# Optimization experiments

Measured on AMD Instinct MI355X. Metric: run time of the kernel, lower is better.

Reference implementation:

```python
import jax, jax.numpy as jnp
import numpy as np

EPS = 1e-12  # matches torch.nn.functional.normalize eps


def _l2_normalize(x):
    n = jnp.linalg.norm(x, axis=-1, keepdims=True)
    return x / jnp.maximum(n, EPS)


def setup_inputs() -> dict:
    key = jax.random.key(0)
    k1, k2, k3, k4 = jax.random.split(key, 4)
    N, D = 8192, 1024
    return {
        "query_ids": jax.random.randint(k1, (N,), 0, 1000, dtype=jnp.int64 if jax.config.jax_enable_x64 else jnp.int32),
        "key_ids": jax.random.randint(k2, (N,), 0, 1000, dtype=jnp.int64 if jax.config.jax_enable_x64 else jnp.int32),
        "query_embed": jax.random.normal(k3, (N, D), dtype=jnp.float32),
        "key_embed": jax.random.normal(k4, (N, D), dtype=jnp.float32),
        "k": 5,
    }


def reference(query_ids, key_ids, query_embed, key_embed, k):
    q = _l2_normalize(query_embed)          # [N, D]
    kb = _l2_normalize(key_embed)           # [N, D]
    sims = q @ kb.T                          # [N, N] cosine similarities
    # argsort(descending)[1:k+1] == top-(k+1) indices, dropping the best match
    _, idx = jax.lax.top_k(sims, k + 1)      # [N, k+1]
    idx = idx[:, 1:]                         # [N, k]
    matched = (key_ids[idx] == query_ids[:, None]).astype(jnp.float32)  # [N, k]
    # mean over k per row, then mean over rows == global mean (equal row sizes)
    return jnp.mean(matched)
```

## Files before the change

kernel.cpp:

```cpp
#include <hip/hip_runtime.h>
#include <math.h>

#define NROWS 8192
#define DIM   1024
#define KDIM  1024
#define KSEL  5
#define TOPK  6
#define QB    128
#define KBB   256
#define NKB   (NROWS / KBB)
#define NQB   (NROWS / QB)
#define PS    51

typedef __attribute__((ext_vector_type(8))) short bf16x8;
typedef __attribute__((ext_vector_type(4))) float f32x4;


__device__ __forceinline__ unsigned short f2bf(float x) {
    unsigned u = __float_as_uint(x);
    unsigned r = (u + 0x7fffu + ((u >> 16) & 1u)) >> 16;
    return (unsigned short)r;
}

__device__ __forceinline__ bool better(float v, int id, float v2, int id2) {
    return (v > v2) || (v == v2 && id < id2);
}
__device__ __forceinline__ void insert6(float v, int id, float* tv, int* ti) {
    if (!better(v, id, tv[TOPK - 1], ti[TOPK - 1])) return;
    int j = TOPK - 1;
    while (j > 0 && better(v, id, tv[j - 1], ti[j - 1])) {
        tv[j] = tv[j - 1]; ti[j] = ti[j - 1]; --j;
    }
    tv[j] = v; ti[j] = id;
}

__device__ __forceinline__ void ins6(float v, int id, float* tv, int* ti) {
    if (v <= tv[5]) return;
    bool gt[6];
#pragma unroll
    for (int j = 0; j < 6; ++j) gt[j] = v > tv[j];
#pragma unroll
    for (int j = 5; j >= 1; --j)
        if (gt[j - 1]) { tv[j] = tv[j - 1]; ti[j] = ti[j - 1]; }
    if (gt[0]) { tv[0] = v; ti[0] = id; }
#pragma unroll
    for (int j = 1; j < 6; ++j)
        if (gt[j] && !gt[j - 1]) { tv[j] = v; ti[j] = id; }
}

__device__ __forceinline__ void async16(const unsigned short* g, unsigned short* l) {
    __builtin_amdgcn_global_load_lds(
        (const __attribute__((address_space(1))) void*)g,
        (__attribute__((address_space(3))) void*)l, 16, 0, 0);
}

__global__ __launch_bounds__(128) void prep_kernel(
        const float* __restrict__ q, const float* __restrict__ kb,
        unsigned short* __restrict__ Q2, unsigned short* __restrict__ K2) {
    const int b = blockIdx.x;
    const bool isQ = (b < NROWS);
    const int r = isQ ? b : b - NROWS;
    const float* src = (isQ ? q : kb) + (size_t)r * DIM;
    unsigned short* D = (isQ ? Q2 : K2) + (size_t)r * KDIM;

    const int t = threadIdx.x;
    float4 v0 = *(const float4*)(src + t * 4);
    float4 v1 = *(const float4*)(src + 512 + t * 4);
    float s = v0.x * v0.x + v0.y * v0.y + v0.z * v0.z + v0.w * v0.w
            + v1.x * v1.x + v1.y * v1.y + v1.z * v1.z + v1.w * v1.w;
    for (int o = 32; o; o >>= 1) s += __shfl_down(s, o, 64);
    __shared__ float wsum[2];
    __shared__ float inv_s;
    int lane = t & 63, wid = t >> 6;
    if (lane == 0) wsum[wid] = s;
    __syncthreads();
    if (t == 0)
        inv_s = 1.0f / fmaxf(sqrtf(wsum[0] + wsum[1]), 1e-12f);
    __syncthreads();
    const float inv = inv_s;

    float xs[8] = {v0.x * inv, v0.y * inv, v0.z * inv, v0.w * inv,
                   v1.x * inv, v1.y * inv, v1.z * inv, v1.w * inv};
    bf16x8 hi;
#pragma unroll
    for (int i = 0; i < 8; ++i)
        hi[i] = (short)f2bf(xs[i]);
    const int off = (t >> 3) * 64 + (((t & 7) ^ (r & 7)) * 8);
    *(bf16x8*)(D + off) = hi;
}

__global__ __launch_bounds__(256, 2) void gemm_topk_kernel(
        const unsigned short* __restrict__ Q2, const unsigned short* __restrict__ K2,
        float2* __restrict__ partials) {
    __shared__ __align__(16) char smem[53248];
    unsigned short* Ks = (unsigned short*)smem;
    unsigned short* Qs = Ks + KBB * 64;
    float2* mbuf = (float2*)smem;

    const int tid = threadIdx.x;
    const int w = tid >> 6, l = tid & 63;
    const int l15 = l & 15, l4 = l >> 4;
    const int qbase = blockIdx.x * QB;
    const int kbase = blockIdx.y * KBB;
    const int wkh = w & 1;
    const int wqh = w >> 1;

    const int arow  = tid >> 3;
    const int akoff = (tid & 7) * 8;

    const int xr = l15 & 7;
    const int fa_row = (wkh * 128 + l15) * 64;
    const int fb_row = (wqh * 64 + l15) * 64;

    const size_t qstage = (size_t)(qbase + arow) * KDIM + akoff;
    const size_t kstage = (size_t)(kbase + arow) * KDIM + akoff;

    f32x4 acc[8][4];
#pragma unroll
    for (int mt = 0; mt < 8; ++mt)
#pragma unroll
        for (int nt = 0; nt < 4; ++nt) acc[mt][nt] = (f32x4){0.f, 0.f, 0.f, 0.f};

#pragma unroll 1
    for (int k0 = 0; k0 < KDIM; k0 += 64) {
#pragma unroll
        for (int j = 0; j < 8; ++j)
            async16(K2 + kstage + (size_t)j * 32 * KDIM + k0,
                    Ks + (tid + j * 256) * 8);
#pragma unroll
        for (int j = 0; j < 4; ++j)
            async16(Q2 + qstage + (size_t)j * 32 * KDIM + k0,
                    Qs + (tid + j * 256) * 8);
        __syncthreads();
#pragma unroll
        for (int ks = 0; ks < 2; ++ks) {
            const int p8 = ((ks * 4 + l4) ^ xr) * 8;
            bf16x8 af[8], bf[4];
#pragma unroll
            for (int mt = 0; mt < 8; ++mt)
                af[mt] = *(const bf16x8*)(Ks + fa_row + mt * 1024 + p8);
#pragma unroll
            for (int nt = 0; nt < 4; ++nt)
                bf[nt] = *(const bf16x8*)(Qs + fb_row + nt * 1024 + p8);
#pragma unroll
            for (int mt = 0; mt < 8; ++mt)
#pragma unroll
                for (int nt = 0; nt < 4; ++nt)
                    acc[mt][nt] = __builtin_amdgcn_mfma_f32_16x16x32_bf16(
                        af[mt], bf[nt], acc[mt][nt], 0, 0, 0);
        }
        __syncthreads();
    }

    float tvl[4][6]; int til[4][6];
#pragma unroll
    for (int n = 0; n < 4; ++n)
#pragma unroll
        for (int i = 0; i < 6; ++i) { tvl[n][i] = -INFINITY; til[n][i] = 0x7fffffff; }

#pragma unroll
    for (int nt = 0; nt < 4; ++nt) {
#pragma unroll
        for (int mt = 0; mt < 8; ++mt) {
            const f32x4 a = acc[mt][nt];
            const float m4 = fmaxf(fmaxf(a.x, a.y), fmaxf(a.z, a.w));
            if (m4 > tvl[nt][5]) {
                const int kk = kbase + wkh * 128 + mt * 16 + l4 * 4;
                ins6(a.x, kk + 0, tvl[nt], til[nt]);
                ins6(a.y, kk + 1, tvl[nt], til[nt]);
                ins6(a.z, kk + 2, tvl[nt], til[nt]);
                ins6(a.w, kk + 3, tvl[nt], til[nt]);
            }
        }
    }

    __syncthreads();
    const int slot = wkh * 4 + l4;
#pragma unroll
    for (int nt = 0; nt < 4; ++nt) {
        const int ql = wqh * 64 + nt * 16 + l15;
        float2* dst = mbuf + (size_t)ql * PS + slot * 6;
#pragma unroll
        for (int e = 0; e < 6; ++e)
            dst[e] = make_float2(tvl[nt][e], __int_as_float(til[nt][e]));
    }
    __syncthreads();

    if (tid < 128) {
        float tv[6]; int ti[6];
#pragma unroll
        for (int i = 0; i < 6; ++i) { tv[i] = -INFINITY; ti[i] = 0x7fffffff; }
        const float2* src = mbuf + (size_t)tid * PS;
        for (int e = 0; e < 48; ++e) {
            float2 p = src[e];
            if (p.x < tv[5]) continue;
            insert6(p.x, __float_as_int(p.y), tv, ti);
        }
        size_t off = ((size_t)(qbase + tid) * NKB + blockIdx.y) * TOPK;
#pragma unroll
        for (int i = 0; i < 6; ++i)
            partials[off + i] = make_float2(tv[i], __int_as_float(ti[i]));
    }
}

__global__ __launch_bounds__(256) void merge_kernel(
        const float2* __restrict__ partials,
        const int* __restrict__ query_ids, const int* __restrict__ key_ids,
        int* __restrict__ counter, int* __restrict__ done,
        float* __restrict__ out) {
    __shared__ float2 lbuf[32][49];
    __shared__ int sc[32];
    const int tid  = threadIdx.x;
    const int rloc = tid >> 3;
    const int part = tid & 7;
    const int row  = blockIdx.x * 32 + rloc;

    float tv[6]; int ti[6];
#pragma unroll
    for (int i = 0; i < 6; ++i) { tv[i] = -INFINITY; ti[i] = 0x7fffffff; }
    const float2* src = partials + ((size_t)row * NKB + part * 4) * TOPK;
#pragma unroll
    for (int e = 0; e < 24; ++e) {
        float2 p = src[e];
        if (p.x < tv[5]) continue;
        insert6(p.x, __float_as_int(p.y), tv, ti);
    }
#pragma unroll
    for (int i = 0; i < 6; ++i)
        lbuf[rloc][part * 6 + i] = make_float2(tv[i], __int_as_float(ti[i]));
    __syncthreads();

    if (part == 0) {
        float tv2[6]; int ti2[6];
#pragma unroll
        for (int i = 0; i < 6; ++i) { tv2[i] = -INFINITY; ti2[i] = 0x7fffffff; }
#pragma unroll
        for (int e = 0; e < 48; ++e) {
            float2 p = lbuf[rloc][e];
            if (p.x < tv2[5]) continue;
            insert6(p.x, __float_as_int(p.y), tv2, ti2);
        }
        const int qid = query_ids[row];
        int cnt = 0;
#pragma unroll
        for (int r = 1; r < TOPK; ++r)
            cnt += (key_ids[ti2[r]] == qid) ? 1 : 0;
        sc[rloc] = cnt;
    }
    __syncthreads();
    if (tid == 0) {
        int c = 0;
#pragma unroll
        for (int i = 0; i < 32; ++i) c += sc[i];
        atomicAdd(counter, c);
        __threadfence();
        int prev = atomicAdd(done, 1);
        if (prev == gridDim.x - 1) {
            int total = atomicAdd(counter, 0);
            out[0] = (float)total / (float)(NROWS * KSEL);
        }
    }
}

extern "C" void kernel_launch(void* const* d_in, const int* in_sizes, int n_in,
                              void* d_out, int out_size, void* d_ws, size_t ws_size,
                              hipStream_t stream) {
    (void)in_sizes; (void)n_in; (void)out_size; (void)ws_size;
    const int*   query_ids = (const int*)d_in[0];
    const int*   key_ids   = (const int*)d_in[1];
    const float* q         = (const float*)d_in[2];
    const float* kb        = (const float*)d_in[3];

    char* ws = (char*)d_ws;
    const size_t MB16 = (size_t)NROWS * KDIM * sizeof(unsigned short);
    int*            counter  = (int*)ws;
    unsigned short* Q2       = (unsigned short*)(ws + 256);
    unsigned short* K2       = (unsigned short*)(ws + 256 + MB16);
    float2*         partials = (float2*)(ws + 256 + 2 * MB16);

    hipMemsetAsync(counter, 0, 2 * sizeof(int), stream);
    prep_kernel<<<2 * NROWS, 128, 0, stream>>>(q, kb, Q2, K2);
    gemm_topk_kernel<<<dim3(NQB, NKB), 256, 0, stream>>>(Q2, K2, partials);
    merge_kernel<<<NROWS / 32, 256, 0, stream>>>(partials, query_ids, key_ids,
                                                 counter, counter + 1,
                                                 (float*)d_out);
}
```

Baseline: 350.8 us.

## Double-buffer LDS tiles with 256-row query block and 512 threads

The query tile per block doubles to 256 rows, run by 512 threads (8 waves). Shared memory becomes two 64KB ping-pong buffers, so the next k-slice's async loads are issued before the MFMA work on the current slice, and one barrier per iteration is removed. MFMA sections are wrapped in s_setprio to favour matrix issue. The 128KB LDS footprint allows at most one block per CU, so latency hiding now relies on the overlap within a block rather than on multiple resident blocks.

```diff
diff --git a/kernel.cpp b/kernel.cpp
--- a/kernel.cpp
+++ b/kernel.cpp
@@ -6,7 +6,7 @@
 #define KDIM  1024
 #define KSEL  5
 #define TOPK  6
-#define QB    128
+#define QB    256
 #define KBB   256
 #define NKB   (NROWS / KBB)
 #define NQB   (NROWS / QB)
@@ -89,12 +89,10 @@
     *(bf16x8*)(D + off) = hi;
 }
 
-__global__ __launch_bounds__(256, 2) void gemm_topk_kernel(
+__global__ __launch_bounds__(512, 2) void gemm_topk_kernel(
         const unsigned short* __restrict__ Q2, const unsigned short* __restrict__ K2,
         float2* __restrict__ partials) {
-    __shared__ __align__(16) char smem[53248];
-    unsigned short* Ks = (unsigned short*)smem;
-    unsigned short* Qs = Ks + KBB * 64;
+    __shared__ __align__(16) char smem[131072];
     float2* mbuf = (float2*)smem;
 
     const int tid = threadIdx.x;
@@ -121,35 +119,62 @@
 #pragma unroll
         for (int nt = 0; nt < 4; ++nt) acc[mt][nt] = (f32x4){0.f, 0.f, 0.f, 0.f};
 
+    {
+        unsigned short* Ksb = (unsigned short*)smem;
+        unsigned short* Qsb = Ksb + 16384;
+#pragma unroll
+        for (int j = 0; j < 4; ++j)
+            async16(K2 + kstage + (size_t)j * 64 * KDIM,
+                    Ksb + (tid + j * 512) * 8);
+#pragma unroll
+        for (int j = 0; j < 4; ++j)
+            async16(Q2 + qstage + (size_t)j * 64 * KDIM,
+                    Qsb + (tid + j * 512) * 8);
+    }
+    __syncthreads();
+
+    int cur = 0;
 #pragma unroll 1
     for (int k0 = 0; k0 < KDIM; k0 += 64) {
-#pragma unroll
-        for (int j = 0; j < 8; ++j)
-            async16(K2 + kstage + (size_t)j * 32 * KDIM + k0,
-                    Ks + (tid + j * 256) * 8);
-#pragma unroll
-        for (int j = 0; j < 4; ++j)
-            async16(Q2 + qstage + (size_t)j * 32 * KDIM + k0,
-                    Qs + (tid + j * 256) * 8);
-        __syncthreads();
+        unsigned short* Ksb = (unsigned short*)(smem + (cur << 16));
+        unsigned short* Qsb = Ksb + 16384;
+
+        const int nk0 = k0 + 64;
+        if (nk0 < KDIM) {
+            unsigned short* Ksn = (unsigned short*)(smem + ((cur ^ 1) << 16));
+            unsigned short* Qsn = Ksn + 16384;
+#pragma unroll
+            for (int j = 0; j < 4; ++j)
+                async16(K2 + kstage + (size_t)j * 64 * KDIM + nk0,
+                        Ksn + (tid + j * 512) * 8);
+#pragma unroll
+            for (int j = 0; j < 4; ++j)
+                async16(Q2 + qstage + (size_t)j * 64 * KDIM + nk0,
+                        Qsn + (tid + j * 512) * 8);
+        }
+
 #pragma unroll
         for (int ks = 0; ks < 2; ++ks) {
             const int p8 = ((ks * 4 + l4) ^ xr) * 8;
-            bf16x8 af[8], bf[4];
+            bf16x8 af[8], bfr[4];
 #pragma unroll
             for (int mt = 0; mt < 8; ++mt)
-                af[mt] = *(const bf16x8*)(Ks + fa_row + mt * 1024 + p8);
+                af[mt] = *(const bf16x8*)(Ksb + fa_row + mt * 1024 + p8);
 #pragma unroll
             for (int nt = 0; nt < 4; ++nt)
-                bf[nt] = *(const bf16x8*)(Qs + fb_row + nt * 1024 + p8);
+                bfr[nt] = *(const bf16x8*)(Qsb + fb_row + nt * 1024 + p8);
+            __builtin_amdgcn_s_setprio(1);
 #pragma unroll
             for (int mt = 0; mt < 8; ++mt)
 #pragma unroll
                 for (int nt = 0; nt < 4; ++nt)
                     acc[mt][nt] = __builtin_amdgcn_mfma_f32_16x16x32_bf16(
-                        af[mt], bf[nt], acc[mt][nt], 0, 0, 0);
-        }
+                        af[mt], bfr[nt], acc[mt][nt], 0, 0, 0);
+            __builtin_amdgcn_s_setprio(0);
+        }
+
         __syncthreads();
+        cur ^= 1;
     }
 
     float tvl[4][6]; int til[4][6];
@@ -186,7 +211,7 @@
     }
     __syncthreads();
 
-    if (tid < 128) {
+    if (tid < 256) {
         float tv[6]; int ti[6];
 #pragma unroll
         for (int i = 0; i < 6; ++i) { tv[i] = -INFINITY; ti[i] = 0x7fffffff; }
@@ -280,7 +305,7 @@
 
     hipMemsetAsync(counter, 0, 2 * sizeof(int), stream);
     prep_kernel<<<2 * NROWS, 128, 0, stream>>>(q, kb, Q2, K2);
-    gemm_topk_kernel<<<dim3(NQB, NKB), 256, 0, stream>>>(Q2, K2, partials);
+    gemm_topk_kernel<<<dim3(NQB, NKB), 512, 0, stream>>>(Q2, K2, partials);
     merge_kernel<<<NROWS / 32, 256, 0, stream>>>(partials, query_ids, key_ids,
                                                  counter, counter + 1,
                                                  (float*)d_out);
```

Measured after the change: 353.2 us. No clear change (+0.7%).

## Double-buffer K tiles, load Q fragments directly to registers, widen GEMM block

Applied to the files above, without the earlier changes.

The GEMM kernel moves to 512 threads covering 256 queries per block. K tiles are double-buffered in LDS with async loads for the next k-step issued before the current MFMAs. Q fragments are fetched straight from global memory into registers one step ahead, dropping the Q LDS staging. MFMA issue is wrapped with s_setprio, and the top-k reduction now runs in two halves. The prep kernel processes one row per wave with no block-level sync. This aims to hide global-load latency and cut LDS traffic, at the cost of more registers and uncoalesced-ish direct global Q loads.

```diff
diff --git a/kernel.cpp b/kernel.cpp
--- a/kernel.cpp
+++ b/kernel.cpp
@@ -6,10 +6,11 @@
 #define KDIM  1024
 #define KSEL  5
 #define TOPK  6
-#define QB    128
+#define QB    256
 #define KBB   256
 #define NKB   (NROWS / KBB)
 #define NQB   (NROWS / QB)
+#define NT    (KDIM / 64)
 #define PS    51
 
 typedef __attribute__((ext_vector_type(8))) short bf16x8;
@@ -54,47 +55,50 @@
         (__attribute__((address_space(3))) void*)l, 16, 0, 0);
 }
 
-__global__ __launch_bounds__(128) void prep_kernel(
+__global__ __launch_bounds__(256) void prep_kernel(
         const float* __restrict__ q, const float* __restrict__ kb,
         unsigned short* __restrict__ Q2, unsigned short* __restrict__ K2) {
-    const int b = blockIdx.x;
+    const int w = threadIdx.x >> 6, lane = threadIdx.x & 63;
+    const int b = blockIdx.x * 4 + w;
     const bool isQ = (b < NROWS);
     const int r = isQ ? b : b - NROWS;
     const float* src = (isQ ? q : kb) + (size_t)r * DIM;
     unsigned short* D = (isQ ? Q2 : K2) + (size_t)r * KDIM;
 
-    const int t = threadIdx.x;
-    float4 v0 = *(const float4*)(src + t * 4);
-    float4 v1 = *(const float4*)(src + 512 + t * 4);
-    float s = v0.x * v0.x + v0.y * v0.y + v0.z * v0.z + v0.w * v0.w
-            + v1.x * v1.x + v1.y * v1.y + v1.z * v1.z + v1.w * v1.w;
+    float4 v[4];
+#pragma unroll
+    for (int i = 0; i < 4; ++i)
+        v[i] = *(const float4*)(src + i * 256 + lane * 4);
+
+    float s = 0.f;
+#pragma unroll
+    for (int i = 0; i < 4; ++i)
+        s += v[i].x * v[i].x + v[i].y * v[i].y + v[i].z * v[i].z + v[i].w * v[i].w;
     for (int o = 32; o; o >>= 1) s += __shfl_down(s, o, 64);
-    __shared__ float wsum[2];
-    __shared__ float inv_s;
-    int lane = t & 63, wid = t >> 6;
-    if (lane == 0) wsum[wid] = s;
-    __syncthreads();
-    if (t == 0)
-        inv_s = 1.0f / fmaxf(sqrtf(wsum[0] + wsum[1]), 1e-12f);
-    __syncthreads();
-    const float inv = inv_s;
-
-    float xs[8] = {v0.x * inv, v0.y * inv, v0.z * inv, v0.w * inv,
-                   v1.x * inv, v1.y * inv, v1.z * inv, v1.w * inv};
-    bf16x8 hi;
-#pragma unroll
-    for (int i = 0; i < 8; ++i)
-        hi[i] = (short)f2bf(xs[i]);
-    const int off = (t >> 3) * 64 + (((t & 7) ^ (r & 7)) * 8);
-    *(bf16x8*)(D + off) = hi;
-}
-
-__global__ __launch_bounds__(256, 2) void gemm_topk_kernel(
+    s = __shfl(s, 0, 64);
+    const float inv = 1.0f / fmaxf(sqrtf(s), 1e-12f);
+
+    bf16x8 g0, g1;
+    g0[0] = (short)f2bf(v[0].x * inv); g0[1] = (short)f2bf(v[0].y * inv);
+    g0[2] = (short)f2bf(v[0].z * inv); g0[3] = (short)f2bf(v[0].w * inv);
+    g0[4] = (short)f2bf(v[2].x * inv); g0[5] = (short)f2bf(v[2].y * inv);
+    g0[6] = (short)f2bf(v[2].z * inv); g0[7] = (short)f2bf(v[2].w * inv);
+    g1[0] = (short)f2bf(v[1].x * inv); g1[1] = (short)f2bf(v[1].y * inv);
+    g1[2] = (short)f2bf(v[1].z * inv); g1[3] = (short)f2bf(v[1].w * inv);
+    g1[4] = (short)f2bf(v[3].x * inv); g1[5] = (short)f2bf(v[3].y * inv);
+    g1[6] = (short)f2bf(v[3].z * inv); g1[7] = (short)f2bf(v[3].w * inv);
+
+    const int perm = ((lane & 7) ^ (r & 7)) * 8;
+    const int off0 = (lane >> 3) * 64 + perm;
+    const int off1 = (8 + (lane >> 3)) * 64 + perm;
+    *(bf16x8*)(D + off0) = g0;
+    *(bf16x8*)(D + off1) = g1;
+}
+
+__global__ __launch_bounds__(512, 2) void gemm_topk_kernel(
         const unsigned short* __restrict__ Q2, const unsigned short* __restrict__ K2,
         float2* __restrict__ partials) {
-    __shared__ __align__(16) char smem[53248];
-    unsigned short* Ks = (unsigned short*)smem;
-    unsigned short* Qs = Ks + KBB * 64;
+    __shared__ __align__(16) char smem[65536];
     float2* mbuf = (float2*)smem;
 
     const int tid = threadIdx.x;
@@ -105,15 +109,20 @@
     const int wkh = w & 1;
     const int wqh = w >> 1;
 
-    const int arow  = tid >> 3;
     const int akoff = (tid & 7) * 8;
-
     const int xr = l15 & 7;
     const int fa_row = (wkh * 128 + l15) * 64;
-    const int fb_row = (wqh * 64 + l15) * 64;
-
-    const size_t qstage = (size_t)(qbase + arow) * KDIM + akoff;
-    const size_t kstage = (size_t)(kbase + arow) * KDIM + akoff;
+
+    const size_t kstage = (size_t)(kbase + (tid >> 3)) * KDIM + akoff;
+
+    unsigned qv[2][4];
+#pragma unroll
+    for (int ks = 0; ks < 2; ++ks)
+#pragma unroll
+        for (int nt = 0; nt < 4; ++nt) {
+            const int qrow = qbase + wqh * 64 + nt * 16 + l15;
+            qv[ks][nt] = (unsigned)qrow * KDIM + (unsigned)(((ks * 4 + l4) ^ xr) * 8);
+        }
 
     f32x4 acc[8][4];
 #pragma unroll
@@ -121,36 +130,73 @@
 #pragma unroll
         for (int nt = 0; nt < 4; ++nt) acc[mt][nt] = (f32x4){0.f, 0.f, 0.f, 0.f};
 
+    unsigned short* Kb0 = (unsigned short*)smem;
+    unsigned short* Kb1 = (unsigned short*)(smem + 32768);
+
+    bf16x8 b0[2][4], b1[2][4];
+
+#pragma unroll
+    for (int j = 0; j < 4; ++j)
+        async16(K2 + kstage + (size_t)j * 64 * KDIM, Kb0 + (tid + j * 512) * 8);
+#pragma unroll
+    for (int ks = 0; ks < 2; ++ks)
+#pragma unroll
+        for (int nt = 0; nt < 4; ++nt)
+            b0[ks][nt] = *(const bf16x8*)(Q2 + qv[ks][nt]);
+    __syncthreads();
+
+#define STEP(TT, CURBUF, NXTBUF, BC, BN)                                      \
+    {                                                                         \
+        const int tt = (TT);                                                  \
+        if (tt + 1 < NT) {                                                    \
+            const size_t nk0 = (size_t)(tt + 1) * 64;                         \
+            _Pragma("unroll")                                                 \
+            for (int j = 0; j < 4; ++j)                                       \
+                async16(K2 + kstage + (size_t)j * 64 * KDIM + nk0,            \
+                        (NXTBUF) + (tid + j * 512) * 8);                      \
+            _Pragma("unroll")                                                 \
+            for (int ks = 0; ks < 2; ++ks)                                    \
+                _Pragma("unroll")                                             \
+                for (int nt = 0; nt < 4; ++nt)                                \
+                    (BN)[ks][nt] = *(const bf16x8*)(Q2 + qv[ks][nt] +         \
+                                                    (unsigned)(tt + 1) * 64); \
+        }                                                                     \
+        _Pragma("unroll")                                                     \
+        for (int ks = 0; ks < 2; ++ks) {                                      \
+            const int p8 = ((ks * 4 + l4) ^ xr) * 8;                          \
+            bf16x8 af[4];                                                     \
+            _Pragma("unroll")                                                 \
+            for (int m = 0; m < 4; ++m)                                       \
+                af[m] = *(const bf16x8*)((CURBUF) + fa_row + m * 1024 + p8);  \
+            __builtin_amdgcn_s_setprio(1);                                    \
+            _Pragma("unroll")                                                 \
+            for (int m = 0; m < 4; ++m)                                       \
+                _Pragma("unroll")                                             \
+                for (int nt = 0; nt < 4; ++nt)                                \
+                    acc[m][nt] = __builtin_amdgcn_mfma_f32_16x16x32_bf16(     \
+                        af[m], (BC)[ks][nt], acc[m][nt], 0, 0, 0);            \
+            __builtin_amdgcn_s_setprio(0);                                    \
+            _Pragma("unroll")                                                 \
+            for (int m = 0; m < 4; ++m)                                       \
+                af[m] = *(const bf16x8*)((CURBUF) + fa_row + (m + 4) * 1024 + p8); \
+            __builtin_amdgcn_s_setprio(1);                                    \
+            _Pragma("unroll")                                                 \
+            for (int m = 0; m < 4; ++m)                                       \
+                _Pragma("unroll")                                             \
+                for (int nt = 0; nt < 4; ++nt)                                \
+                    acc[m + 4][nt] = __builtin_amdgcn_mfma_f32_16x16x32_bf16( \
+                        af[m], (BC)[ks][nt], acc[m + 4][nt], 0, 0, 0);        \
+            __builtin_amdgcn_s_setprio(0);                                    \
+        }                                                                     \
+        __syncthreads();        \
+    }
+
 #pragma unroll 1
-    for (int k0 = 0; k0 < KDIM; k0 += 64) {
-#pragma unroll
-        for (int j = 0; j < 8; ++j)
-            async16(K2 + kstage + (size_t)j * 32 * KDIM + k0,
-                    Ks + (tid + j * 256) * 8);
-#pragma unroll
-        for (int j = 0; j < 4; ++j)
-            async16(Q2 + qstage + (size_t)j * 32 * KDIM + k0,
-                    Qs + (tid + j * 256) * 8);
-        __syncthreads();
-#pragma unroll
-        for (int ks = 0; ks < 2; ++ks) {
-            const int p8 = ((ks * 4 + l4) ^ xr) * 8;
-            bf16x8 af[8], bf[4];
-#pragma unroll
-            for (int mt = 0; mt < 8; ++mt)
-                af[mt] = *(const bf16x8*)(Ks + fa_row + mt * 1024 + p8);
-#pragma unroll
-            for (int nt = 0; nt < 4; ++nt)
-                bf[nt] = *(const bf16x8*)(Qs + fb_row + nt * 1024 + p8);
-#pragma unroll
-            for (int mt = 0; mt < 8; ++mt)
-#pragma unroll
-                for (int nt = 0; nt < 4; ++nt)
-                    acc[mt][nt] = __builtin_amdgcn_mfma_f32_16x16x32_bf16(
-                        af[mt], bf[nt], acc[mt][nt], 0, 0, 0);
-        }
-        __syncthreads();
-    }
+    for (int t2 = 0; t2 < NT; t2 += 2) {
+        STEP(t2,     Kb0, Kb1, b0, b1);
+        STEP(t2 + 1, Kb1, Kb0, b1, b0);
+    }
+#undef STEP
 
     float tvl[4][6]; int til[4][6];
 #pragma unroll
@@ -174,32 +220,36 @@
         }
     }
 
-    __syncthreads();
     const int slot = wkh * 4 + l4;
-#pragma unroll
-    for (int nt = 0; nt < 4; ++nt) {
-        const int ql = wqh * 64 + nt * 16 + l15;
-        float2* dst = mbuf + (size_t)ql * PS + slot * 6;
-#pragma unroll
-        for (int e = 0; e < 6; ++e)
-            dst[e] = make_float2(tvl[nt][e], __int_as_float(til[nt][e]));
-    }
-    __syncthreads();
-
-    if (tid < 128) {
-        float tv[6]; int ti[6];
-#pragma unroll
-        for (int i = 0; i < 6; ++i) { tv[i] = -INFINITY; ti[i] = 0x7fffffff; }
-        const float2* src = mbuf + (size_t)tid * PS;
-        for (int e = 0; e < 48; ++e) {
-            float2 p = src[e];
-            if (p.x < tv[5]) continue;
-            insert6(p.x, __float_as_int(p.y), tv, ti);
-        }
-        size_t off = ((size_t)(qbase + tid) * NKB + blockIdx.y) * TOPK;
-#pragma unroll
-        for (int i = 0; i < 6; ++i)
-            partials[off + i] = make_float2(tv[i], __int_as_float(ti[i]));
+#pragma unroll 1
+    for (int h = 0; h < 2; ++h) {
+        if ((wqh >> 1) == h) {
+#pragma unroll
+            for (int nt = 0; nt < 4; ++nt) {
+                const int ql = (wqh & 1) * 64 + nt * 16 + l15;
+                float2* dst = mbuf + (size_t)ql * PS + slot * 6;
+#pragma unroll
+                for (int e = 0; e < 6; ++e)
+                    dst[e] = make_float2(tvl[nt][e], __int_as_float(til[nt][e]));
+            }
+        }
+        __syncthreads();
+        if (tid < 128) {
+            float tv[6]; int ti[6];
+#pragma unroll
+            for (int i = 0; i < 6; ++i) { tv[i] = -INFINITY; ti[i] = 0x7fffffff; }
+            const float2* src = mbuf + (size_t)tid * PS;
+            for (int e = 0; e < 48; ++e) {
+                float2 p = src[e];
+                if (p.x < tv[5]) continue;
+                insert6(p.x, __float_as_int(p.y), tv, ti);
+            }
+            size_t off = ((size_t)(qbase + h * 128 + tid) * NKB + blockIdx.y) * TOPK;
+#pragma unroll
+            for (int i = 0; i < 6; ++i)
+                partials[off + i] = make_float2(tv[i], __int_as_float(ti[i]));
+        }
+        __syncthreads();
     }
 }
 
@@ -279,8 +329,8 @@
     float2*         partials = (float2*)(ws + 256 + 2 * MB16);
 
     hipMemsetAsync(counter, 0, 2 * sizeof(int), stream);
-    prep_kernel<<<2 * NROWS, 128, 0, stream>>>(q, kb, Q2, K2);
-    gemm_topk_kernel<<<dim3(NQB, NKB), 256, 0, stream>>>(Q2, K2, partials);
+    prep_kernel<<<(2 * NROWS) / 4, 256, 0, stream>>>(q, kb, Q2, K2);
+    gemm_topk_kernel<<<dim3(NQB, NKB), 512, 0, stream>>>(Q2, K2, partials);
     merge_kernel<<<NROWS / 32, 256, 0, stream>>>(partials, query_ids, key_ids,
                                                  counter, counter + 1,
                                                  (float*)d_out);
```

After: 731.5 us. +108.5%, slower.

## Load GEMM fragments directly from global memory, drop LDS staging and barriers

Applied to the files above, without the earlier changes.

The GEMM main loop no longer stages Q and K tiles into shared memory with async loads and block barriers. Each wave now reads its bf16 MFMA fragments straight from global memory through L2/L1, and raises wave priority around the MFMA bursts. The prep kernel is also reworked so one wave normalizes one row, which removes the shared-memory reduction and its syncthreads. The trade is that operands once shared through LDS are now re-read from cache by several waves, and global-load latency is exposed per k-step with no software pipelining.

```diff
diff --git a/kernel.cpp b/kernel.cpp
--- a/kernel.cpp
+++ b/kernel.cpp
@@ -10,6 +10,7 @@
 #define KBB   256
 #define NKB   (NROWS / KBB)
 #define NQB   (NROWS / QB)
+#define NT    (KDIM / 64)
 #define PS    51
 
 typedef __attribute__((ext_vector_type(8))) short bf16x8;
@@ -48,54 +49,50 @@
         if (gt[j] && !gt[j - 1]) { tv[j] = v; ti[j] = id; }
 }
 
-__device__ __forceinline__ void async16(const unsigned short* g, unsigned short* l) {
-    __builtin_amdgcn_global_load_lds(
-        (const __attribute__((address_space(1))) void*)g,
-        (__attribute__((address_space(3))) void*)l, 16, 0, 0);
-}
-
-__global__ __launch_bounds__(128) void prep_kernel(
+__global__ __launch_bounds__(256) void prep_kernel(
         const float* __restrict__ q, const float* __restrict__ kb,
         unsigned short* __restrict__ Q2, unsigned short* __restrict__ K2) {
-    const int b = blockIdx.x;
+    const int w = threadIdx.x >> 6, lane = threadIdx.x & 63;
+    const int b = blockIdx.x * 4 + w;
     const bool isQ = (b < NROWS);
     const int r = isQ ? b : b - NROWS;
     const float* src = (isQ ? q : kb) + (size_t)r * DIM;
     unsigned short* D = (isQ ? Q2 : K2) + (size_t)r * KDIM;
 
-    const int t = threadIdx.x;
-    float4 v0 = *(const float4*)(src + t * 4);
-    float4 v1 = *(const float4*)(src + 512 + t * 4);
-    float s = v0.x * v0.x + v0.y * v0.y + v0.z * v0.z + v0.w * v0.w
-            + v1.x * v1.x + v1.y * v1.y + v1.z * v1.z + v1.w * v1.w;
+    float4 v[4];
+#pragma unroll
+    for (int i = 0; i < 4; ++i)
+        v[i] = *(const float4*)(src + i * 256 + lane * 4);
+
+    float s = 0.f;
+#pragma unroll
+    for (int i = 0; i < 4; ++i)
+        s += v[i].x * v[i].x + v[i].y * v[i].y + v[i].z * v[i].z + v[i].w * v[i].w;
     for (int o = 32; o; o >>= 1) s += __shfl_down(s, o, 64);
-    __shared__ float wsum[2];
-    __shared__ float inv_s;
-    int lane = t & 63, wid = t >> 6;
-    if (lane == 0) wsum[wid] = s;
-    __syncthreads();
-    if (t == 0)
-        inv_s = 1.0f / fmaxf(sqrtf(wsum[0] + wsum[1]), 1e-12f);
-    __syncthreads();
-    const float inv = inv_s;
-
-    float xs[8] = {v0.x * inv, v0.y * inv, v0.z * inv, v0.w * inv,
-                   v1.x * inv, v1.y * inv, v1.z * inv, v1.w * inv};
-    bf16x8 hi;
-#pragma unroll
-    for (int i = 0; i < 8; ++i)
-        hi[i] = (short)f2bf(xs[i]);
-    const int off = (t >> 3) * 64 + (((t & 7) ^ (r & 7)) * 8);
-    *(bf16x8*)(D + off) = hi;
+    s = __shfl(s, 0, 64);
+    const float inv = 1.0f / fmaxf(sqrtf(s), 1e-12f);
+
+    bf16x8 g0, g1;
+    g0[0] = (short)f2bf(v[0].x * inv); g0[1] = (short)f2bf(v[0].y * inv);
+    g0[2] = (short)f2bf(v[0].z * inv); g0[3] = (short)f2bf(v[0].w * inv);
+    g0[4] = (short)f2bf(v[2].x * inv); g0[5] = (short)f2bf(v[2].y * inv);
+    g0[6] = (short)f2bf(v[2].z * inv); g0[7] = (short)f2bf(v[2].w * inv);
+    g1[0] = (short)f2bf(v[1].x * inv); g1[1] = (short)f2bf(v[1].y * inv);
+    g1[2] = (short)f2bf(v[1].z * inv); g1[3] = (short)f2bf(v[1].w * inv);
+    g1[4] = (short)f2bf(v[3].x * inv); g1[5] = (short)f2bf(v[3].y * inv);
+    g1[6] = (short)f2bf(v[3].z * inv); g1[7] = (short)f2bf(v[3].w * inv);
+
+    const int perm = ((lane & 7) ^ (r & 7)) * 8;
+    const int off0 = (lane >> 3) * 64 + perm;
+    const int off1 = (8 + (lane >> 3)) * 64 + perm;
+    *(bf16x8*)(D + off0) = g0;
+    *(bf16x8*)(D + off1) = g1;
 }
 
 __global__ __launch_bounds__(256, 2) void gemm_topk_kernel(
         const unsigned short* __restrict__ Q2, const unsigned short* __restrict__ K2,
         float2* __restrict__ partials) {
-    __shared__ __align__(16) char smem[53248];
-    unsigned short* Ks = (unsigned short*)smem;
-    unsigned short* Qs = Ks + KBB * 64;
-    float2* mbuf = (float2*)smem;
+    __shared__ float2 mbuf[128 * PS];
 
     const int tid = threadIdx.x;
     const int w = tid >> 6, l = tid & 63;
@@ -104,16 +101,15 @@
     const int kbase = blockIdx.y * KBB;
     const int wkh = w & 1;
     const int wqh = w >> 1;
-
-    const int arow  = tid >> 3;
-    const int akoff = (tid & 7) * 8;
-
     const int xr = l15 & 7;
-    const int fa_row = (wkh * 128 + l15) * 64;
-    const int fb_row = (wqh * 64 + l15) * 64;
-
-    const size_t qstage = (size_t)(qbase + arow) * KDIM + akoff;
-    const size_t kstage = (size_t)(kbase + arow) * KDIM + akoff;
+
+    const unsigned kof = (unsigned)(kbase + wkh * 128 + l15) * KDIM;
+    unsigned qof[4];
+#pragma unroll
+    for (int nt = 0; nt < 4; ++nt)
+        qof[nt] = (unsigned)(qbase + wqh * 64 + nt * 16 + l15) * KDIM;
+    const unsigned pe0 = (unsigned)((l4 ^ xr) * 8);
+    const unsigned pe1 = (unsigned)(((4 + l4) ^ xr) * 8);
 
     f32x4 acc[8][4];
 #pragma unroll
@@ -122,34 +118,28 @@
         for (int nt = 0; nt < 4; ++nt) acc[mt][nt] = (f32x4){0.f, 0.f, 0.f, 0.f};
 
 #pragma unroll 1
-    for (int k0 = 0; k0 < KDIM; k0 += 64) {
-#pragma unroll
-        for (int j = 0; j < 8; ++j)
-            async16(K2 + kstage + (size_t)j * 32 * KDIM + k0,
-                    Ks + (tid + j * 256) * 8);
-#pragma unroll
-        for (int j = 0; j < 4; ++j)
-            async16(Q2 + qstage + (size_t)j * 32 * KDIM + k0,
-                    Qs + (tid + j * 256) * 8);
-        __syncthreads();
-#pragma unroll
+    for (int t = 0; t < NT; ++t) {
+        const unsigned tb = (unsigned)t * 64u;
+#pragma unroll 1
         for (int ks = 0; ks < 2; ++ks) {
-            const int p8 = ((ks * 4 + l4) ^ xr) * 8;
-            bf16x8 af[8], bf[4];
+            const unsigned pk = tb + (ks ? pe1 : pe0);
+            bf16x8 bq[4];
+#pragma unroll
+            for (int nt = 0; nt < 4; ++nt)
+                bq[nt] = *(const bf16x8*)(Q2 + qof[nt] + pk);
+            bf16x8 af[8];
 #pragma unroll
             for (int mt = 0; mt < 8; ++mt)
-                af[mt] = *(const bf16x8*)(Ks + fa_row + mt * 1024 + p8);
-#pragma unroll
-            for (int nt = 0; nt < 4; ++nt)
-                bf[nt] = *(const bf16x8*)(Qs + fb_row + nt * 1024 + p8);
+                af[mt] = *(const bf16x8*)(K2 + kof + (unsigned)mt * (16u * KDIM) + pk);
+            __builtin_amdgcn_s_setprio(1);
 #pragma unroll
             for (int mt = 0; mt < 8; ++mt)
 #pragma unroll
                 for (int nt = 0; nt < 4; ++nt)
                     acc[mt][nt] = __builtin_amdgcn_mfma_f32_16x16x32_bf16(
-                        af[mt], bf[nt], acc[mt][nt], 0, 0, 0);
-        }
-        __syncthreads();
+                        af[mt], bq[nt], acc[mt][nt], 0, 0, 0);
+            __builtin_amdgcn_s_setprio(0);
+        }
     }
 
     float tvl[4][6]; int til[4][6];
@@ -174,7 +164,6 @@
         }
     }
 
-    __syncthreads();
     const int slot = wkh * 4 + l4;
 #pragma unroll
     for (int nt = 0; nt < 4; ++nt) {
@@ -279,7 +268,7 @@
     float2*         partials = (float2*)(ws + 256 + 2 * MB16);
 
     hipMemsetAsync(counter, 0, 2 * sizeof(int), stream);
-    prep_kernel<<<2 * NROWS, 128, 0, stream>>>(q, kb, Q2, K2);
+    prep_kernel<<<(2 * NROWS) / 4, 256, 0, stream>>>(q, kb, Q2, K2);
     gemm_topk_kernel<<<dim3(NQB, NKB), 256, 0, stream>>>(Q2, K2, partials);
     merge_kernel<<<NROWS / 32, 256, 0, stream>>>(partials, query_ids, key_ids,
                                                  counter, counter + 1,
```

Result: slower. 367.2 us (+4.7%).
